# Performance work log

Hardware: AMD Instinct MI355X
Metric: run time of the kernel (lower is better)

Reference implementation:

```python
import jax, jax.numpy as jnp
import numpy as np

B, T, D, U = 16, 8192, 256, 256


def setup_inputs() -> dict:
    key = jax.random.key(0)
    k1, k2, k3, k4, k5 = jax.random.split(key, 5)
    scale = 1.0 / np.sqrt(D)
    return {
        "query": jax.random.normal(k1, (B, D), dtype=jnp.float32),
        "value": jax.random.normal(k2, (B, T, D), dtype=jnp.float32),
        "W1": jax.random.normal(k3, (D, U), dtype=jnp.float32) * scale,
        "W2": jax.random.normal(k4, (D, U), dtype=jnp.float32) * scale,
        "V": jax.random.normal(k5, (U, 1), dtype=jnp.float32) * scale,
    }


def reference(query, value, W1, W2, V):
    # query: [B, D], value: [B, T, D]
    # additive (Bahdanau) attention:
    #   score_t = V^T tanh(W1 value_t + W2 query)
    hidden = jnp.einsum('bd,du->bu', query, W2)[:, None, :]       # [B, 1, U]
    keys = jnp.einsum('btd,du->btu', value, W1)                   # [B, T, U]
    score = jnp.einsum('btu,uo->bto', jnp.tanh(keys + hidden), V) # [B, T, 1]
    attention_weights = jax.nn.softmax(score, axis=1)             # over time
    context_vector = jnp.sum(attention_weights * value, axis=1)   # [B, D]
    return context_vector
```

## Files before the change

kernel.cpp:

```cpp
#include <hip/hip_runtime.h>
#include <cstdint>
#include <cstddef>

#define B_ 16
#define T_ 8192
#define D_ 256
#define U_ 256

typedef __attribute__((ext_vector_type(8))) short bf16x8;
typedef __attribute__((ext_vector_type(4))) float f32x4;
typedef __attribute__((ext_vector_type(4))) unsigned int u32x4;

__device__ inline f32x4 mfma16(bf16x8 a, bf16x8 b, f32x4 c) {
    return __builtin_amdgcn_mfma_f32_16x16x32_bf16(a, b, c, 0, 0, 0);
}

__device__ inline unsigned int pack2_hi(float x, float y) {
    return __builtin_amdgcn_perm(__float_as_uint(y), __float_as_uint(x), 0x07060302u);
}
__device__ inline float lo_part(float x) {
    return x - __uint_as_float(__float_as_uint(x) & 0xffff0000u);
}

__device__ inline void cvt8(const float* __restrict__ p, bf16x8& hi, bf16x8& lo) {
    const float4 a = *reinterpret_cast<const float4*>(p);
    const float4 b = *reinterpret_cast<const float4*>(p + 4);
    u32x4 h, l;
    h[0] = pack2_hi(a.x, a.y);
    h[1] = pack2_hi(a.z, a.w);
    h[2] = pack2_hi(b.x, b.y);
    h[3] = pack2_hi(b.z, b.w);
    l[0] = pack2_hi(lo_part(a.x), lo_part(a.y));
    l[1] = pack2_hi(lo_part(a.z), lo_part(a.w));
    l[2] = pack2_hi(lo_part(b.x), lo_part(b.y));
    l[3] = pack2_hi(lo_part(b.z), lo_part(b.w));
    hi = __builtin_bit_cast(bf16x8, h);
    lo = __builtin_bit_cast(bf16x8, l);
}

__global__ __launch_bounds__(256) void prep_w1t_kernel(const float* __restrict__ W1,
                                                       unsigned short* __restrict__ hi,
                                                       unsigned short* __restrict__ lo) {
    const int idx = blockIdx.x * 256 + threadIdx.x;
    const int d = idx >> 8;
    const int u = idx & 255;
    const float x = W1[idx];
    const unsigned int xb = __float_as_uint(x);
    const unsigned short h = (unsigned short)(xb >> 16);
    const float lf = x - __uint_as_float(xb & 0xffff0000u);
    const unsigned short lo16 = (unsigned short)(__float_as_uint(lf) >> 16);
    hi[u * D_ + d] = h;
    lo[u * D_ + d] = lo16;
}

__global__ __launch_bounds__(256) void hidden_kernel(const float* __restrict__ q,
                                                     const float* __restrict__ W2,
                                                     float* __restrict__ hidden) {
    const int b = blockIdx.x;
    const int u = threadIdx.x;
    __shared__ float qs[D_];
    qs[u] = q[b * D_ + u];
    __syncthreads();
    float acc = 0.f;
#pragma unroll 8
    for (int d = 0; d < D_; ++d)
        acc += qs[d] * W2[d * U_ + u];
    hidden[b * U_ + u] = acc;
}

__global__ __launch_bounds__(256, 2) void scores_ctx_kernel(
        const float* __restrict__ value,
        const unsigned short* __restrict__ w1t_hi,
        const unsigned short* __restrict__ w1t_lo,
        const float* __restrict__ Vv,
        const float* __restrict__ hidden,
        float* __restrict__ partial,
        float* __restrict__ mstat,
        float* __restrict__ lstat) {
    const int b    = blockIdx.y;
    const int bx   = blockIdx.x;
    const int t0   = bx * 128;
    const int tid  = threadIdx.x;
    const int w    = tid >> 6;
    const int lane = tid & 63;
    const int lr   = lane & 15;
    const int lk   = lane >> 4;

    __shared__ unsigned short bhi[2][256 * 32];
    __shared__ unsigned short blo[2][256 * 32];
    __shared__ float s_lds[128];
    __shared__ float e_lds[128];
    __shared__ float redm[4];
    __shared__ float redl[4];

    const int srow = (lane >> 2);
    const int scol = (lane & 3) * 8;
    auto stage_b = [&](int bf, int k0) {
#pragma unroll
        for (int i = 0; i < 4; ++i) {
            const unsigned short* g = w1t_hi + (size_t)(w * 64 + i * 16 + srow) * D_ + k0 + scol;
            __builtin_amdgcn_global_load_lds(
                (const __attribute__((address_space(1))) void*)g,
                (__attribute__((address_space(3))) void*)&bhi[bf][(w * 64 + i * 16) * 32],
                16, 0, 0);
        }
#pragma unroll
        for (int i = 0; i < 4; ++i) {
            const unsigned short* g = w1t_lo + (size_t)(w * 64 + i * 16 + srow) * D_ + k0 + scol;
            __builtin_amdgcn_global_load_lds(
                (const __attribute__((address_space(1))) void*)g,
                (__attribute__((address_space(3))) void*)&blo[bf][(w * 64 + i * 16) * 32],
                16, 0, 0);
        }
    };

    f32x4 acc[2][16] = {};
    const float* aptr = value + ((size_t)b * T_ + t0 + w * 32 + lr) * D_ + lk * 8;

    stage_b(0, 0);
    __syncthreads();

    int cur = 0;
    for (int k = 0; k < 8; ++k) {
        const int k0 = k << 5;
        if (k < 7) stage_b(cur ^ 1, k0 + 32);

        bf16x8 ah[2], al[2];
#pragma unroll
        for (int tf = 0; tf < 2; ++tf)
            cvt8(aptr + (size_t)tf * 16 * D_ + k0, ah[tf], al[tf]);

#pragma unroll
        for (int uf = 0; uf < 16; ++uf) {
            const bf16x8 bh = *reinterpret_cast<const bf16x8*>(&bhi[cur][(uf * 16 + lr) * 32 + lk * 8]);
            const bf16x8 bl = *reinterpret_cast<const bf16x8*>(&blo[cur][(uf * 16 + lr) * 32 + lk * 8]);
#pragma unroll
            for (int tf = 0; tf < 2; ++tf) {
                acc[tf][uf] = mfma16(ah[tf], bh, acc[tf][uf]);
                acc[tf][uf] = mfma16(al[tf], bh, acc[tf][uf]);
                acc[tf][uf] = mfma16(ah[tf], bl, acc[tf][uf]);
            }
        }
        __syncthreads();
        cur ^= 1;
    }

    float hv[16], vwv[16];
#pragma unroll
    for (int uf = 0; uf < 16; ++uf) {
        const int u = uf * 16 + lr;
        hv[uf]  = hidden[b * U_ + u];
        vwv[uf] = Vv[u];
    }
#pragma unroll
    for (int tf = 0; tf < 2; ++tf) {
#pragma unroll
        for (int r = 0; r < 4; ++r) {
            float p = 0.f;
#pragma unroll
            for (int uf = 0; uf < 16; ++uf) {
                const float z = acc[tf][uf][r] + hv[uf];
                const float e = __expf(2.f * z);
                p += (1.f - __fdividef(2.f, e + 1.f)) * vwv[uf];
            }
            p += __shfl_xor(p, 1, 64);
            p += __shfl_xor(p, 2, 64);
            p += __shfl_xor(p, 4, 64);
            p += __shfl_xor(p, 8, 64);
            if (lr == 0) s_lds[w * 32 + tf * 16 + lk * 4 + r] = p;
        }
    }
    __syncthreads();

    float x = (tid < 128) ? s_lds[tid] : -3e38f;
#pragma unroll
    for (int m = 1; m < 64; m <<= 1) x = fmaxf(x, __shfl_xor(x, m, 64));
    if (lane == 0) redm[w] = x;
    __syncthreads();
    const float mc = fmaxf(fmaxf(redm[0], redm[1]), fmaxf(redm[2], redm[3]));

    float e = 0.f;
    if (tid < 128) {
        e = __expf(s_lds[tid] - mc);
        e_lds[tid] = e;
    }
    float l = e;
#pragma unroll
    for (int m = 1; m < 64; m <<= 1) l += __shfl_xor(l, m, 64);
    if (lane == 0) redl[w] = l;
    __syncthreads();
    const float lc = redl[0] + redl[1] + redl[2] + redl[3];

    const float* vb = value + ((size_t)b * T_ + t0) * D_ + tid;
    float a0 = 0.f, a1 = 0.f;
#pragma unroll 8
    for (int t = 0; t < 128; t += 2) {
        a0 += e_lds[t]     * vb[(size_t)t * D_];
        a1 += e_lds[t + 1] * vb[(size_t)(t + 1) * D_];
    }
    partial[((size_t)b * 64 + bx) * D_ + tid] = a0 + a1;
    if (tid == 0) {
        mstat[b * 64 + bx] = mc;
        lstat[b * 64 + bx] = lc;
    }
}

__global__ __launch_bounds__(256) void combine_kernel(const float* __restrict__ partial,
                                                      const float* __restrict__ mstat,
                                                      const float* __restrict__ lstat,
                                                      float* __restrict__ out) {
    const int b = blockIdx.x;
    const int d = threadIdx.x;
    float M = -3e38f;
#pragma unroll 8
    for (int c = 0; c < 64; ++c) M = fmaxf(M, mstat[b * 64 + c]);
    float L = 0.f, a = 0.f;
#pragma unroll 4
    for (int c = 0; c < 64; ++c) {
        const float s = __expf(mstat[b * 64 + c] - M);
        L += lstat[b * 64 + c] * s;
        a += s * partial[((size_t)b * 64 + c) * D_ + d];
    }
    out[b * D_ + d] = a / L;
}

extern "C" void kernel_launch(void* const* d_in, const int* in_sizes, int n_in,
                              void* d_out, int out_size, void* d_ws, size_t ws_size,
                              hipStream_t stream) {
    const float* q     = (const float*)d_in[0];
    const float* value = (const float*)d_in[1];
    const float* W1    = (const float*)d_in[2];
    const float* W2    = (const float*)d_in[3];
    const float* Vv    = (const float*)d_in[4];
    float* out = (float*)d_out;

    char* ws = (char*)d_ws;
    unsigned short* w1t_hi  = (unsigned short*)(ws);
    unsigned short* w1t_lo  = (unsigned short*)(ws + 131072);
    float*          hidden  = (float*)(ws + 262144);
    float*          partial = (float*)(ws + 278528);
    float*          mstat   = (float*)(ws + 1327104);
    float*          lstat   = (float*)(ws + 1331200);

    prep_w1t_kernel<<<dim3(256), dim3(256), 0, stream>>>(W1, w1t_hi, w1t_lo);
    hidden_kernel<<<dim3(B_), dim3(256), 0, stream>>>(q, W2, hidden);

    dim3 g2(T_ / 128, B_);
    scores_ctx_kernel<<<g2, dim3(256), 0, stream>>>(value, w1t_hi, w1t_lo, Vv, hidden,
                                                    partial, mstat, lstat);

    combine_kernel<<<dim3(B_), dim3(256), 0, stream>>>(partial, mstat, lstat, out);
}
```

Before: 102.9 us.

## Split U dimension across wave pairs with 512-thread blocks in scores kernel

The score/context kernel now runs 8 waves per block. Each pair of waves shares a 32-row time slice and splits the 256 U columns in half, so per-wave accumulators drop from 32 to 16 MFMA tiles. The goal is lower register pressure and more resident waves per CU to hide latency. Partial scores from the two halves are summed through LDS, and the context accumulation splits time across two thread halves with an extra LDS reduction. In exchange, each wave pair redundantly loads and converts the same value rows, and there is one more barrier.

```diff
diff --git a/kernel.cpp b/kernel.cpp
--- a/kernel.cpp
+++ b/kernel.cpp
@@ -68,7 +68,7 @@
     hidden[b * U_ + u] = acc;
 }
 
-__global__ __launch_bounds__(256, 2) void scores_ctx_kernel(
+__global__ __launch_bounds__(512, 4) void scores_ctx_kernel(
         const float* __restrict__ value,
         const unsigned short* __restrict__ w1t_hi,
         const unsigned short* __restrict__ w1t_lo,
@@ -85,37 +85,36 @@
     const int lane = tid & 63;
     const int lr   = lane & 15;
     const int lk   = lane >> 4;
-
-    __shared__ unsigned short bhi[2][256 * 32];
-    __shared__ unsigned short blo[2][256 * 32];
-    __shared__ float s_lds[128];
+    const int g    = w >> 1;
+    const int h    = w & 1;
+
+    __shared__ unsigned short bhi[2][16 * 512];
+    __shared__ unsigned short blo[2][16 * 512];
+    __shared__ float s_half[2][128];
     __shared__ float e_lds[128];
-    __shared__ float redm[4];
-    __shared__ float redl[4];
-
-    const int srow = (lane >> 2);
-    const int scol = (lane & 3) * 8;
+    __shared__ float redm[8];
+    __shared__ float redl[8];
+    __shared__ float cpart[256];
+
     auto stage_b = [&](int bf, int k0) {
 #pragma unroll
-        for (int i = 0; i < 4; ++i) {
-            const unsigned short* g = w1t_hi + (size_t)(w * 64 + i * 16 + srow) * D_ + k0 + scol;
+        for (int i = 0; i < 2; ++i) {
+            const int uf = w * 2 + i;
+            const unsigned short* gh = w1t_hi + (size_t)(uf * 16 + lr) * D_ + k0 + lk * 8;
             __builtin_amdgcn_global_load_lds(
-                (const __attribute__((address_space(1))) void*)g,
-                (__attribute__((address_space(3))) void*)&bhi[bf][(w * 64 + i * 16) * 32],
+                (const __attribute__((address_space(1))) void*)gh,
+                (__attribute__((address_space(3))) void*)&bhi[bf][uf * 512],
                 16, 0, 0);
-        }
-#pragma unroll
-        for (int i = 0; i < 4; ++i) {
-            const unsigned short* g = w1t_lo + (size_t)(w * 64 + i * 16 + srow) * D_ + k0 + scol;
+            const unsigned short* gl = w1t_lo + (size_t)(uf * 16 + lr) * D_ + k0 + lk * 8;
             __builtin_amdgcn_global_load_lds(
-                (const __attribute__((address_space(1))) void*)g,
-                (__attribute__((address_space(3))) void*)&blo[bf][(w * 64 + i * 16) * 32],
+                (const __attribute__((address_space(1))) void*)gl,
+                (__attribute__((address_space(3))) void*)&blo[bf][uf * 512],
                 16, 0, 0);
         }
     };
 
-    f32x4 acc[2][16] = {};
-    const float* aptr = value + ((size_t)b * T_ + t0 + w * 32 + lr) * D_ + lk * 8;
+    f32x4 acc[2][8] = {};
+    const float* aptr = value + ((size_t)b * T_ + t0 + g * 32 + lr) * D_ + lk * 8;
 
     stage_b(0, 0);
     __syncthreads();
@@ -131,26 +130,27 @@
             cvt8(aptr + (size_t)tf * 16 * D_ + k0, ah[tf], al[tf]);
 
 #pragma unroll
-        for (int uf = 0; uf < 16; ++uf) {
-            const bf16x8 bh = *reinterpret_cast<const bf16x8*>(&bhi[cur][(uf * 16 + lr) * 32 + lk * 8]);
-            const bf16x8 bl = *reinterpret_cast<const bf16x8*>(&blo[cur][(uf * 16 + lr) * 32 + lk * 8]);
+        for (int ufl = 0; ufl < 8; ++ufl) {
+            const int ufg = h * 8 + ufl;
+            const bf16x8 bh = *reinterpret_cast<const bf16x8*>(&bhi[cur][ufg * 512 + lane * 8]);
+            const bf16x8 bl = *reinterpret_cast<const bf16x8*>(&blo[cur][ufg * 512 + lane * 8]);
 #pragma unroll
             for (int tf = 0; tf < 2; ++tf) {
-                acc[tf][uf] = mfma16(ah[tf], bh, acc[tf][uf]);
-                acc[tf][uf] = mfma16(al[tf], bh, acc[tf][uf]);
-                acc[tf][uf] = mfma16(ah[tf], bl, acc[tf][uf]);
+                acc[tf][ufl] = mfma16(ah[tf], bh, acc[tf][ufl]);
+                acc[tf][ufl] = mfma16(al[tf], bh, acc[tf][ufl]);
+                acc[tf][ufl] = mfma16(ah[tf], bl, acc[tf][ufl]);
             }
         }
         __syncthreads();
         cur ^= 1;
     }
 
-    float hv[16], vwv[16];
-#pragma unroll
-    for (int uf = 0; uf < 16; ++uf) {
-        const int u = uf * 16 + lr;
-        hv[uf]  = hidden[b * U_ + u];
-        vwv[uf] = Vv[u];
+    float hv[8], vwv[8];
+#pragma unroll
+    for (int ufl = 0; ufl < 8; ++ufl) {
+        const int u = h * 128 + ufl * 16 + lr;
+        hv[ufl]  = hidden[b * U_ + u];
+        vwv[ufl] = Vv[u];
     }
 #pragma unroll
     for (int tf = 0; tf < 2; ++tf) {
@@ -158,30 +158,30 @@
         for (int r = 0; r < 4; ++r) {
             float p = 0.f;
 #pragma unroll
-            for (int uf = 0; uf < 16; ++uf) {
-                const float z = acc[tf][uf][r] + hv[uf];
+            for (int ufl = 0; ufl < 8; ++ufl) {
+                const float z = acc[tf][ufl][r] + hv[ufl];
                 const float e = __expf(2.f * z);
-                p += (1.f - __fdividef(2.f, e + 1.f)) * vwv[uf];
+                p += (1.f - __fdividef(2.f, e + 1.f)) * vwv[ufl];
             }
             p += __shfl_xor(p, 1, 64);
             p += __shfl_xor(p, 2, 64);
             p += __shfl_xor(p, 4, 64);
             p += __shfl_xor(p, 8, 64);
-            if (lr == 0) s_lds[w * 32 + tf * 16 + lk * 4 + r] = p;
-        }
-    }
-    __syncthreads();
-
-    float x = (tid < 128) ? s_lds[tid] : -3e38f;
+            if (lr == 0) s_half[h][g * 32 + tf * 16 + lk * 4 + r] = p;
+        }
+    }
+    __syncthreads();
+
+    float x = (tid < 128) ? (s_half[0][tid] + s_half[1][tid]) : -3e38f;
 #pragma unroll
     for (int m = 1; m < 64; m <<= 1) x = fmaxf(x, __shfl_xor(x, m, 64));
     if (lane == 0) redm[w] = x;
     __syncthreads();
-    const float mc = fmaxf(fmaxf(redm[0], redm[1]), fmaxf(redm[2], redm[3]));
+    const float mc = fmaxf(redm[0], redm[1]);
 
     float e = 0.f;
     if (tid < 128) {
-        e = __expf(s_lds[tid] - mc);
+        e = __expf(s_half[0][tid] + s_half[1][tid] - mc);
         e_lds[tid] = e;
     }
     float l = e;
@@ -189,16 +189,25 @@
     for (int m = 1; m < 64; m <<= 1) l += __shfl_xor(l, m, 64);
     if (lane == 0) redl[w] = l;
     __syncthreads();
-    const float lc = redl[0] + redl[1] + redl[2] + redl[3];
-
-    const float* vb = value + ((size_t)b * T_ + t0) * D_ + tid;
-    float a0 = 0.f, a1 = 0.f;
+    const float lc = redl[0] + redl[1];
+
+    {
+        const int half = tid >> 8;
+        const int d    = tid & 255;
+        const float* vb = value + ((size_t)b * T_ + t0 + half * 64) * D_ + d;
+        const float* el = &e_lds[half * 64];
+        float a0 = 0.f, a1 = 0.f;
 #pragma unroll 8
-    for (int t = 0; t < 128; t += 2) {
-        a0 += e_lds[t]     * vb[(size_t)t * D_];
-        a1 += e_lds[t + 1] * vb[(size_t)(t + 1) * D_];
-    }
-    partial[((size_t)b * 64 + bx) * D_ + tid] = a0 + a1;
+        for (int t = 0; t < 64; t += 2) {
+            a0 += el[t]     * vb[(size_t)t * D_];
+            a1 += el[t + 1] * vb[(size_t)(t + 1) * D_];
+        }
+        const float csum = a0 + a1;
+        if (half == 1) cpart[d] = csum;
+        __syncthreads();
+        if (half == 0)
+            partial[((size_t)b * 64 + bx) * D_ + d] = csum + cpart[d];
+    }
     if (tid == 0) {
         mstat[b * 64 + bx] = mc;
         lstat[b * 64 + bx] = lc;
@@ -246,7 +255,7 @@
     hidden_kernel<<<dim3(B_), dim3(256), 0, stream>>>(q, W2, hidden);
 
     dim3 g2(T_ / 128, B_);
-    scores_ctx_kernel<<<g2, dim3(256), 0, stream>>>(value, w1t_hi, w1t_lo, Vv, hidden,
+    scores_ctx_kernel<<<g2, dim3(512), 0, stream>>>(value, w1t_hi, w1t_lo, Vv, hidden,
                                                     partial, mstat, lstat);
 
     combine_kernel<<<dim3(B_), dim3(256), 0, stream>>>(partial, mstat, lstat, out);
```

Result: slower. 125.5 us (+21.9%).

## Prefetch next A tile into registers and store W1 tiles in fragment order

Applied to the files above, without the earlier changes.

The value (A operand) fp32 loads for the next k-step are now issued a full iteration early into registers, so their global latency overlaps the current step's MFMA work instead of stalling right before conversion. The W1 hi/lo LDS tiles are also relaid out in MFMA fragment order (uf*512 + lane*8), so each lane reads a contiguous 16-byte chunk, aiming to avoid LDS bank conflicts from the old row-strided layout. The cost is extra VGPRs for the prefetched float4s, which may pressure occupancy given the large accumulator array.

```diff
diff --git a/kernel.cpp b/kernel.cpp
--- a/kernel.cpp
+++ b/kernel.cpp
@@ -22,9 +22,7 @@
     return x - __uint_as_float(__float_as_uint(x) & 0xffff0000u);
 }
 
-__device__ inline void cvt8(const float* __restrict__ p, bf16x8& hi, bf16x8& lo) {
-    const float4 a = *reinterpret_cast<const float4*>(p);
-    const float4 b = *reinterpret_cast<const float4*>(p + 4);
+__device__ inline void cvt8v(const float4 a, const float4 b, bf16x8& hi, bf16x8& lo) {
     u32x4 h, l;
     h[0] = pack2_hi(a.x, a.y);
     h[1] = pack2_hi(a.z, a.w);
@@ -86,30 +84,26 @@
     const int lr   = lane & 15;
     const int lk   = lane >> 4;
 
-    __shared__ unsigned short bhi[2][256 * 32];
-    __shared__ unsigned short blo[2][256 * 32];
+    __shared__ unsigned short bhi[2][16 * 512];
+    __shared__ unsigned short blo[2][16 * 512];
     __shared__ float s_lds[128];
     __shared__ float e_lds[128];
     __shared__ float redm[4];
     __shared__ float redl[4];
 
-    const int srow = (lane >> 2);
-    const int scol = (lane & 3) * 8;
     auto stage_b = [&](int bf, int k0) {
 #pragma unroll
         for (int i = 0; i < 4; ++i) {
-            const unsigned short* g = w1t_hi + (size_t)(w * 64 + i * 16 + srow) * D_ + k0 + scol;
+            const int uf = w * 4 + i;
+            const unsigned short* gh = w1t_hi + (size_t)(uf * 16 + lr) * D_ + k0 + lk * 8;
             __builtin_amdgcn_global_load_lds(
-                (const __attribute__((address_space(1))) void*)g,
-                (__attribute__((address_space(3))) void*)&bhi[bf][(w * 64 + i * 16) * 32],
+                (const __attribute__((address_space(1))) void*)gh,
+                (__attribute__((address_space(3))) void*)&bhi[bf][uf * 512],
                 16, 0, 0);
-        }
-#pragma unroll
-        for (int i = 0; i < 4; ++i) {
-            const unsigned short* g = w1t_lo + (size_t)(w * 64 + i * 16 + srow) * D_ + k0 + scol;
+            const unsigned short* gl = w1t_lo + (size_t)(uf * 16 + lr) * D_ + k0 + lk * 8;
             __builtin_amdgcn_global_load_lds(
-                (const __attribute__((address_space(1))) void*)g,
-                (__attribute__((address_space(3))) void*)&blo[bf][(w * 64 + i * 16) * 32],
+                (const __attribute__((address_space(1))) void*)gl,
+                (__attribute__((address_space(3))) void*)&blo[bf][uf * 512],
                 16, 0, 0);
         }
     };
@@ -117,23 +111,37 @@
     f32x4 acc[2][16] = {};
     const float* aptr = value + ((size_t)b * T_ + t0 + w * 32 + lr) * D_ + lk * 8;
 
+    float4 a0[2], a1[2];
+#pragma unroll
+    for (int tf = 0; tf < 2; ++tf) {
+        a0[tf] = *reinterpret_cast<const float4*>(aptr + (size_t)tf * 16 * D_);
+        a1[tf] = *reinterpret_cast<const float4*>(aptr + (size_t)tf * 16 * D_ + 4);
+    }
     stage_b(0, 0);
     __syncthreads();
 
     int cur = 0;
     for (int k = 0; k < 8; ++k) {
         const int k0 = k << 5;
-        if (k < 7) stage_b(cur ^ 1, k0 + 32);
+        float4 n0[2], n1[2];
+        if (k < 7) {
+#pragma unroll
+            for (int tf = 0; tf < 2; ++tf) {
+                n0[tf] = *reinterpret_cast<const float4*>(aptr + (size_t)tf * 16 * D_ + k0 + 32);
+                n1[tf] = *reinterpret_cast<const float4*>(aptr + (size_t)tf * 16 * D_ + k0 + 36);
+            }
+            stage_b(cur ^ 1, k0 + 32);
+        }
 
         bf16x8 ah[2], al[2];
 #pragma unroll
         for (int tf = 0; tf < 2; ++tf)
-            cvt8(aptr + (size_t)tf * 16 * D_ + k0, ah[tf], al[tf]);
+            cvt8v(a0[tf], a1[tf], ah[tf], al[tf]);
 
 #pragma unroll
         for (int uf = 0; uf < 16; ++uf) {
-            const bf16x8 bh = *reinterpret_cast<const bf16x8*>(&bhi[cur][(uf * 16 + lr) * 32 + lk * 8]);
-            const bf16x8 bl = *reinterpret_cast<const bf16x8*>(&blo[cur][(uf * 16 + lr) * 32 + lk * 8]);
+            const bf16x8 bh = *reinterpret_cast<const bf16x8*>(&bhi[cur][uf * 512 + lane * 8]);
+            const bf16x8 bl = *reinterpret_cast<const bf16x8*>(&blo[cur][uf * 512 + lane * 8]);
 #pragma unroll
             for (int tf = 0; tf < 2; ++tf) {
                 acc[tf][uf] = mfma16(ah[tf], bh, acc[tf][uf]);
@@ -142,6 +150,8 @@
             }
         }
         __syncthreads();
+#pragma unroll
+        for (int tf = 0; tf < 2; ++tf) { a0[tf] = n0[tf]; a1[tf] = n1[tf]; }
         cur ^= 1;
     }
 
@@ -192,13 +202,13 @@
     const float lc = redl[0] + redl[1] + redl[2] + redl[3];
 
     const float* vb = value + ((size_t)b * T_ + t0) * D_ + tid;
-    float a0 = 0.f, a1 = 0.f;
+    float ca0 = 0.f, ca1 = 0.f;
 #pragma unroll 8
     for (int t = 0; t < 128; t += 2) {
-        a0 += e_lds[t]     * vb[(size_t)t * D_];
-        a1 += e_lds[t + 1] * vb[(size_t)(t + 1) * D_];
-    }
-    partial[((size_t)b * 64 + bx) * D_ + tid] = a0 + a1;
+        ca0 += e_lds[t]     * vb[(size_t)t * D_];
+        ca1 += e_lds[t + 1] * vb[(size_t)(t + 1) * D_];
+    }
+    partial[((size_t)b * 64 + bx) * D_ + tid] = ca0 + ca1;
     if (tid == 0) {
         mstat[b * 64 + bx] = mc;
         lstat[b * 64 + bx] = lc;
```

Measured after the change: 107.8 us. +4.7%, slower.
